# Performance work log

Hardware: AMD Instinct MI355X
Metric: run time of the kernel (lower is better)

Reference implementation:

```python
import jax, jax.numpy as jnp
import numpy as np

B, T, C = 1, 4096, 1024
N_HEAD = 16
HEAD_DIM = C // N_HEAD
SCALE = 1.0 / np.sqrt(HEAD_DIM).astype(np.float32)


def setup_inputs() -> dict:
    key = jax.random.key(0)
    k1, k2, k3 = jax.random.split(key, 3)
    x = jax.random.normal(k1, (B, T, C), dtype=jnp.float32)
    W_attn = jax.random.normal(k2, (C, 3 * C), dtype=jnp.float32) * 0.02
    b_attn = jnp.zeros((3 * C,), dtype=jnp.float32)
    W_proj = jax.random.normal(k3, (C, C), dtype=jnp.float32) * 0.02
    b_proj = jnp.zeros((C,), dtype=jnp.float32)
    return {"x": x, "W_attn": W_attn, "b_attn": b_attn, "W_proj": W_proj, "b_proj": b_proj}


def reference(x, W_attn, b_attn, W_proj, b_proj):
    Bq, Tq, Cq = x.shape
    qkv = x @ W_attn + b_attn                      # [B, T, 3C]
    q, k, v = jnp.split(qkv, 3, axis=-1)
    # split heads -> [B, H, T, D]
    def split_heads(t):
        return t.reshape(Bq, Tq, N_HEAD, HEAD_DIM).transpose(0, 2, 1, 3)
    q, k, v = split_heads(q), split_heads(k), split_heads(v)
    scores = jnp.einsum('bhqd,bhkd->bhqk', q, k) * SCALE  # [B, H, T, T]
    causal = jnp.tril(jnp.ones((Tq, Tq), dtype=bool))
    scores = jnp.where(causal[None, None], scores, jnp.float32(-jnp.inf))
    probs = jax.nn.softmax(scores, axis=-1)
    out = jnp.einsum('bhqk,bhkd->bhqd', probs, v)          # [B, H, T, D]
    out = out.transpose(0, 2, 1, 3).reshape(Bq, Tq, Cq)    # merge heads
    out = out @ W_proj + b_proj
    return out
```

## Files before the change

kernel.cpp:

```cpp
#include <hip/hip_runtime.h>
#include <hip/hip_bf16.h>


typedef unsigned short u16;
typedef u16 u16x4 __attribute__((ext_vector_type(4)));
typedef u16 u16x8 __attribute__((ext_vector_type(8)));
typedef __bf16 bf16x8 __attribute__((ext_vector_type(8)));
typedef float f32x4 __attribute__((ext_vector_type(4)));

#define T_SEQ 4096
#define C_DIM 1024
#define NH 16
#define HD 64
#define QSC 0.18033688f
#define NJOBS 1280

static __device__ __forceinline__ u16 f2bf(float f) {
    __hip_bfloat16 h = __float2bfloat16(f);
    return __builtin_bit_cast(u16, h);
}

static __device__ __forceinline__ bf16x8 ldfr(const u16* base, int byteoff) {
    return __builtin_bit_cast(bf16x8, *(const u16x8*)(base + (byteoff >> 1)));
}

static __device__ __forceinline__ void gld_lds16(const void* g, void* l) {
    __builtin_amdgcn_global_load_lds((const __attribute__((address_space(1))) void*)g,
                                     (__attribute__((address_space(3))) void*)l, 16, 0, 0);
}

#define MFMA16(a, b, c) __builtin_amdgcn_mfma_f32_16x16x32_bf16((a), (b), (c), 0, 0, 0)


__global__ __launch_bounds__(256) void k_cvt_x(const float* __restrict__ x, u16* __restrict__ xb) {
    int i = (blockIdx.x * 256 + threadIdx.x) * 8;
    float4 a = *(const float4*)(x + i);
    float4 b = *(const float4*)(x + i + 4);
    u16x8 o;
    o[0] = f2bf(a.x); o[1] = f2bf(a.y); o[2] = f2bf(a.z); o[3] = f2bf(a.w);
    o[4] = f2bf(b.x); o[5] = f2bf(b.y); o[6] = f2bf(b.z); o[7] = f2bf(b.w);
    *(u16x8*)(xb + i) = o;
}

__global__ __launch_bounds__(256) void k_transpose_w(const float* __restrict__ src,
                                                     u16* __restrict__ dst, int R, int Cc) {
    __shared__ float tile[32][33];
    int bx = blockIdx.x * 32;
    int by = blockIdx.y * 32;
    int x = threadIdx.x, y = threadIdx.y;
#pragma unroll
    for (int i = 0; i < 32; i += 8)
        tile[y + i][x] = src[(by + y + i) * Cc + bx + x];
    __syncthreads();
#pragma unroll
    for (int i = 0; i < 32; i += 8)
        dst[(bx + y + i) * R + by + x] = f2bf(tile[x][y + i]);
}


template <int EPI>
__global__ __launch_bounds__(256) void k_gemm(const u16* __restrict__ A, const u16* __restrict__ Bt,
                                              const float* __restrict__ bias,
                                              u16* __restrict__ outQ, u16* __restrict__ outK,
                                              u16* __restrict__ outVt, float* __restrict__ outF,
                                              int kd, int nbx) {
    __shared__ u16 Al[128 * 64];
    __shared__ u16 Bl[128 * 64];
    const int tid = threadIdx.x;
    const int lane = tid & 63;
    const int wid = tid >> 6;
    const int wm = wid >> 1, wn = wid & 1;
    const int c = lane & 15, g = lane >> 4;
    const int nwg = gridDim.x;
    const int swzb = ((int)blockIdx.x & 7) * (nwg >> 3) + ((int)blockIdx.x >> 3);
    const int m0 = (swzb % nbx) * 128;
    const int n0 = (swzb / nbx) * 128;
    const int srow = lane >> 3;
    const int sxu = (((lane & 7) * 16) ^ (srow << 4)) >> 1;
    const int swa = (c & 7) << 4;

    f32x4 acc[4][4] = {};

    for (int k0 = 0; k0 < kd; k0 += 64) {
#pragma unroll
        for (int i = 0; i < 4; ++i) {
            const int ch = wid * 4 + i;
            const int row = ch * 8 + srow;
            gld_lds16(A + (m0 + row) * kd + k0 + sxu, &Al[ch * 512]);
            gld_lds16(Bt + (n0 + row) * kd + k0 + sxu, &Bl[ch * 512]);
        }
        __syncthreads();
        bf16x8 af[4][2], bfm[4][2];
#pragma unroll
        for (int mi = 0; mi < 4; ++mi) {
            const u16* p = Al + (wm * 64 + mi * 16 + c) * 64;
            af[mi][0] = ldfr(p, (16 * g) ^ swa);
            af[mi][1] = ldfr(p, (64 + 16 * g) ^ swa);
        }
#pragma unroll
        for (int ni = 0; ni < 4; ++ni) {
            const u16* p = Bl + (wn * 64 + ni * 16 + c) * 64;
            bfm[ni][0] = ldfr(p, (16 * g) ^ swa);
            bfm[ni][1] = ldfr(p, (64 + 16 * g) ^ swa);
        }
#pragma unroll
        for (int mi = 0; mi < 4; ++mi)
#pragma unroll
            for (int ni = 0; ni < 4; ++ni) {
                acc[mi][ni] = MFMA16(af[mi][0], bfm[ni][0], acc[mi][ni]);
                acc[mi][ni] = MFMA16(af[mi][1], bfm[ni][1], acc[mi][ni]);
            }
        __syncthreads();
    }

    const int mbase = m0 + wm * 64;
    const int nbase = n0 + wn * 64;
    if (EPI == 0) {
        const int part = m0 >> 10;
#pragma unroll
        for (int mi = 0; mi < 4; ++mi) {
            const int fbase = mbase + mi * 16 + 4 * g;
            const f32x4 bv = *(const f32x4*)(bias + part * 1024 + (part ? fbase - part * 1024 + part * 1024 : fbase));
            const int fr = fbase & 1023;
            const int h = fr >> 6, d0 = fr & 63;
#pragma unroll
            for (int ni = 0; ni < 4; ++ni) {
                const int tok = nbase + ni * 16 + c;
                if (part == 2) {
#pragma unroll
                    for (int r = 0; r < 4; ++r)
                        outVt[(size_t)(fr + r) * T_SEQ + tok] = f2bf(acc[mi][ni][r] + bv[r]);
                } else {
                    u16x4 pk;
#pragma unroll
                    for (int r = 0; r < 4; ++r) {
                        float v = acc[mi][ni][r] + bv[r];
                        pk[r] = f2bf(part == 0 ? v * QSC : v);
                    }
                    u16* dst = (part == 0 ? outQ : outK);
                    *(u16x4*)(dst + (size_t)(h * T_SEQ + tok) * HD + d0) = pk;
                }
            }
        }
    } else {
#pragma unroll
        for (int mi = 0; mi < 4; ++mi) {
            const int fbase = mbase + mi * 16 + 4 * g;
            const f32x4 bv = *(const f32x4*)(bias + fbase);
#pragma unroll
            for (int ni = 0; ni < 4; ++ni) {
                const int tok = nbase + ni * 16 + c;
                f32x4 w;
#pragma unroll
                for (int r = 0; r < 4; ++r) w[r] = acc[mi][ni][r] + bv[r];
                *(f32x4*)(outF + (size_t)tok * C_DIM + fbase) = w;
            }
        }
    }
}


static __device__ __forceinline__ void p_gen(f32x4 s[4], int qabs, int kv0, int g,
                                             bool domask, bf16x8 pa[2]) {
    if (domask) {
#pragma unroll
        for (int tau = 0; tau < 4; ++tau) {
            const int kb = kv0 + 32 * (tau >> 1) + 4 * (tau & 1) + 8 * g;
#pragma unroll
            for (int r = 0; r < 4; ++r)
                if (kb + r > qabs) s[tau][r] = -3e38f;
        }
    }
    u16 pb[4][4];
#pragma unroll
    for (int tau = 0; tau < 4; ++tau)
#pragma unroll
        for (int r = 0; r < 4; ++r)
            pb[tau][r] = f2bf(__builtin_amdgcn_exp2f(s[tau][r]));
    const u16x8 p0 = {pb[0][0], pb[0][1], pb[0][2], pb[0][3], pb[1][0], pb[1][1], pb[1][2], pb[1][3]};
    const u16x8 p1 = {pb[2][0], pb[2][1], pb[2][2], pb[2][3], pb[3][0], pb[3][1], pb[3][2], pb[3][3]};
    pa[0] = __builtin_bit_cast(bf16x8, p0);
    pa[1] = __builtin_bit_cast(bf16x8, p1);
}

__global__ __launch_bounds__(256) void k_flash(const u16* __restrict__ Qg, const u16* __restrict__ Kg,
                                               const u16* __restrict__ Vtg,
                                               float* __restrict__ part, float* __restrict__ lpart,
                                               unsigned* __restrict__ cnt) {
    __shared__ u16 sm[2][2][4096];
    volatile unsigned* jw = (volatile unsigned*)&sm[0][0][0];

    const int tid = threadIdx.x;
    const int lane = tid & 63;
    const int wid = tid >> 6;
    const int c = lane & 15, g = lane >> 4;
    const int srow = lane >> 3;
    const int sxu = (((lane & 7) * 16) ^ (srow << 4)) >> 1;

    const u16x8 onespat = {0x3F80, 0x3F80, 0x3F80, 0x3F80, 0x3F80, 0x3F80, 0x3F80, 0x3F80};
    const bf16x8 onesf = __builtin_bit_cast(bf16x8, onespat);

    for (;;) {
        if (tid == 0) *jw = atomicAdd(cnt, 1u);
        __syncthreads();
        const unsigned j = *jw;
        __syncthreads();
        if (j >= (unsigned)NJOBS) break;

        const int head = (int)(j & 15u);
        const int idx = (int)(j >> 4);
        int qb, ch, nc;
        if (idx < 32)      { qb = 31 - (idx >> 2); ch = idx & 3; nc = 4; }
        else if (idx < 56) { const int t = idx - 32; qb = 23 - t / 3;    ch = t % 3; nc = 3; }
        else if (idx < 72) { const int t = idx - 56; qb = 15 - (t >> 1); ch = t & 1; nc = 2; }
        else               { qb = 7 - (idx - 72); ch = 0; nc = 1; }
        const int ntile = 2 * qb + 2;
        const int cbase = ntile / nc, crem = ntile % nc;
        const int len = cbase + (ch < crem ? 1 : 0);
        const int start = ch * cbase + (ch < crem ? ch : crem);

        const int q0w = qb * 128 + wid * 32;

        const u16* Qh = Qg + (size_t)head * (T_SEQ * HD);
        const u16* Kh = Kg + (size_t)head * (T_SEQ * HD);
        const u16* Vh = Vtg + (size_t)head * (HD * T_SEQ);

        bf16x8 qf[2][2];
#pragma unroll
        for (int h = 0; h < 2; ++h)
#pragma unroll
            for (int dc = 0; dc < 2; ++dc)
                qf[h][dc] = __builtin_bit_cast(
                    bf16x8, *(const u16x8*)(Qh + (q0w + 16 * h + c) * HD + dc * 32 + 8 * g));

        f32x4 o0[4] = {}, o1[4] = {}, ol0 = {}, ol1 = {};

        {
            const int kvs = start * 64;
#pragma unroll
            for (int i = 0; i < 2; ++i) {
                const int chk = wid * 2 + i;
                gld_lds16(Kh + (kvs + chk * 8 + srow) * HD + sxu, &sm[0][0][chk * 512]);
                gld_lds16(Vh + (chk * 8 + srow) * T_SEQ + kvs + sxu, &sm[0][1][chk * 512]);
            }
        }
        __syncthreads();

        for (int t = 0; t < len; ++t) {
            const int cur = t & 1;
            const int kv0 = (start + t) * 64;
            if (t + 1 < len) {
                const int kvn = kv0 + 64;
#pragma unroll
                for (int i = 0; i < 2; ++i) {
                    const int chk = wid * 2 + i;
                    gld_lds16(Kh + (kvn + chk * 8 + srow) * HD + sxu, &sm[cur ^ 1][0][chk * 512]);
                    gld_lds16(Vh + (chk * 8 + srow) * T_SEQ + kvn + sxu, &sm[cur ^ 1][1][chk * 512]);
                }
            }
            const u16* Kl = &sm[cur][0][0];
            const u16* Vl = &sm[cur][1][0];
            f32x4 s0[4], s1[4];
            __builtin_amdgcn_s_setprio(1);
#pragma unroll
            for (int tau = 0; tau < 4; ++tau) {
                const int prow = 32 * (tau >> 1) + 4 * (tau & 1) + 8 * (c >> 2) + (c & 3);
                const int sw = (prow & 7) << 4;
                const u16* kb = Kl + prow * 64;
                const bf16x8 k0 = ldfr(kb, (16 * g) ^ sw);
                const bf16x8 k1 = ldfr(kb, (64 + 16 * g) ^ sw);
                f32x4 z0 = {}, z1 = {};
                z0 = MFMA16(k0, qf[0][0], z0);
                s0[tau] = MFMA16(k1, qf[0][1], z0);
                z1 = MFMA16(k0, qf[1][0], z1);
                s1[tau] = MFMA16(k1, qf[1][1], z1);
            }
            __builtin_amdgcn_s_setprio(0);
            const bool dm0 = (kv0 + 63) > (q0w);
            const bool dm1 = (kv0 + 63) > (q0w + 16);
            bf16x8 pa0[2], pa1[2];
            p_gen(s0, q0w + c, kv0, g, dm0, pa0);
            p_gen(s1, q0w + 16 + c, kv0, g, dm1, pa1);
            const int swv = (c & 7) << 4;
            __builtin_amdgcn_s_setprio(1);
#pragma unroll
            for (int n = 0; n < 4; ++n) {
                const u16* vb = Vl + (n * 16 + c) * 64;
                const bf16x8 v0 = ldfr(vb, (16 * g) ^ swv);
                const bf16x8 v1 = ldfr(vb, (64 + 16 * g) ^ swv);
                o0[n] = MFMA16(v0, pa0[0], o0[n]);
                o0[n] = MFMA16(v1, pa0[1], o0[n]);
                o1[n] = MFMA16(v0, pa1[0], o1[n]);
                o1[n] = MFMA16(v1, pa1[1], o1[n]);
            }
            ol0 = MFMA16(onesf, pa0[0], ol0);
            ol0 = MFMA16(onesf, pa0[1], ol0);
            ol1 = MFMA16(onesf, pa1[0], ol1);
            ol1 = MFMA16(onesf, pa1[1], ol1);
            __builtin_amdgcn_s_setprio(0);
            __syncthreads();
        }

        float* slot = part + (size_t)j * 8192u;
        float* lsl = lpart + (size_t)j * 128u;
        const int ql0 = wid * 32 + c;
#pragma unroll
        for (int n = 0; n < 4; ++n) {
            *(f32x4*)(slot + ql0 * 64 + n * 16 + 4 * g) = o0[n];
            *(f32x4*)(slot + (ql0 + 16) * 64 + n * 16 + 4 * g) = o1[n];
        }
        if (g == 0) {
            lsl[ql0] = ol0[0];
            lsl[ql0 + 16] = ol1[0];
        }
        __syncthreads();
    }
}


__global__ __launch_bounds__(256) void k_combine(const float* __restrict__ part,
                                                 const float* __restrict__ lpart,
                                                 u16* __restrict__ Ab) {
    const int head = blockIdx.x >> 5, qb = blockIdx.x & 31;
    int nc, idx0;
    if (qb >= 24)      { nc = 4; idx0 = (31 - qb) * 4; }
    else if (qb >= 16) { nc = 3; idx0 = 32 + (23 - qb) * 3; }
    else if (qb >= 8)  { nc = 2; idx0 = 56 + (15 - qb) * 2; }
    else               { nc = 1; idx0 = 72 + (7 - qb); }

    const int q = threadIdx.x >> 1;
    const int dh = (threadIdx.x & 1) * 32;
    f32x4 a[8] = {};
    float l = 0.f;
    for (int i = 0; i < nc; ++i) {
        const unsigned jj = (unsigned)(((idx0 + i) << 4) | head);
        const float* sp = part + (size_t)jj * 8192u + q * 64 + dh;
#pragma unroll
        for (int r = 0; r < 8; ++r) a[r] += *(const f32x4*)(sp + 4 * r);
        l += lpart[(size_t)jj * 128u + q];
    }
    const float li = 1.0f / l;
    u16* dst = Ab + (size_t)(qb * 128 + q) * C_DIM + head * HD + dh;
#pragma unroll
    for (int v = 0; v < 4; ++v) {
        u16x8 w;
#pragma unroll
        for (int r = 0; r < 4; ++r) {
            w[r] = f2bf(a[2 * v][r] * li);
            w[r + 4] = f2bf(a[2 * v + 1][r] * li);
        }
        *(u16x8*)(dst + v * 8) = w;
    }
}


extern "C" void kernel_launch(void* const* d_in, const int* in_sizes, int n_in,
                              void* d_out, int out_size, void* d_ws, size_t ws_size,
                              hipStream_t stream) {
    const float* x      = (const float*)d_in[0];
    const float* W_attn = (const float*)d_in[1];
    const float* b_attn = (const float*)d_in[2];
    const float* W_proj = (const float*)d_in[3];
    const float* b_proj = (const float*)d_in[4];
    float* out = (float*)d_out;

    char* ws = (char*)d_ws;
    u16* xb    = (u16*)(ws);
    u16* Wat   = (u16*)(ws + (8u << 20));
    u16* Wpt   = (u16*)(ws + (14u << 20));
    u16* Qb    = (u16*)(ws + (16u << 20));
    u16* Kb    = (u16*)(ws + (24u << 20));
    u16* Vtb   = (u16*)(ws + (32u << 20));
    float* prt = (float*)(ws + (40u << 20));
    float* lpt = (float*)(ws + (80u << 20));
    u16* Ab    = xb;

    unsigned* cnt = (unsigned*)d_out;
    hipMemsetAsync(cnt, 0, 4, stream);

    k_cvt_x<<<2048, 256, 0, stream>>>(x, xb);
    k_transpose_w<<<dim3(96, 32), dim3(32, 8), 0, stream>>>(W_attn, Wat, 1024, 3072);
    k_transpose_w<<<dim3(32, 32), dim3(32, 8), 0, stream>>>(W_proj, Wpt, 1024, 1024);
    k_gemm<0><<<768, 256, 0, stream>>>(Wat, xb, b_attn, Qb, Kb, Vtb, nullptr, 1024, 24);
    k_flash<<<640, 256, 0, stream>>>(Qb, Kb, Vtb, prt, lpt, cnt);
    k_combine<<<512, 256, 0, stream>>>(prt, lpt, Ab);
    k_gemm<1><<<256, 256, 0, stream>>>(Wpt, Ab, b_proj, nullptr, nullptr, nullptr, out, 1024, 8);
}
```

Baseline: 166.2 us.

## Split flash attention into finer KV chunks and store bf16 partials

Raises the number of split-KV jobs from 1280 to 2304, using up to 8 chunks per query block, and doubles the persistent flash grid. The goal is better load balance and more work in flight across CUs. Partial outputs are now stored as bf16 instead of fp32, which halves the write and read traffic between the flash and combine kernels. In exchange, the combine step has more partials to sum, and rounding the unnormalized partials to bf16 adds precision loss. The bias indexing expression is also simplified.

```diff
diff --git a/kernel.cpp b/kernel.cpp
--- a/kernel.cpp
+++ b/kernel.cpp
@@ -13,11 +13,15 @@
 #define NH 16
 #define HD 64
 #define QSC 0.18033688f
-#define NJOBS 1280
+#define NJOBS 2304
 
 static __device__ __forceinline__ u16 f2bf(float f) {
     __hip_bfloat16 h = __float2bfloat16(f);
     return __builtin_bit_cast(u16, h);
+}
+
+static __device__ __forceinline__ float bf2f(u16 u) {
+    return __builtin_bit_cast(float, (unsigned)u << 16);
 }
 
 static __device__ __forceinline__ bf16x8 ldfr(const u16* base, int byteoff) {
@@ -120,7 +124,7 @@
 #pragma unroll
         for (int mi = 0; mi < 4; ++mi) {
             const int fbase = mbase + mi * 16 + 4 * g;
-            const f32x4 bv = *(const f32x4*)(bias + part * 1024 + (part ? fbase - part * 1024 + part * 1024 : fbase));
+            const f32x4 bv = *(const f32x4*)(bias + fbase);
             const int fr = fbase & 1023;
             const int h = fr >> 6, d0 = fr & 63;
 #pragma unroll
@@ -185,7 +189,7 @@
 
 __global__ __launch_bounds__(256) void k_flash(const u16* __restrict__ Qg, const u16* __restrict__ Kg,
                                                const u16* __restrict__ Vtg,
-                                               float* __restrict__ part, float* __restrict__ lpart,
+                                               u16* __restrict__ part, float* __restrict__ lpart,
                                                unsigned* __restrict__ cnt) {
     __shared__ u16 sm[2][2][4096];
     volatile unsigned* jw = (volatile unsigned*)&sm[0][0][0];
@@ -210,10 +214,14 @@
         const int head = (int)(j & 15u);
         const int idx = (int)(j >> 4);
         int qb, ch, nc;
-        if (idx < 32)      { qb = 31 - (idx >> 2); ch = idx & 3; nc = 4; }
-        else if (idx < 56) { const int t = idx - 32; qb = 23 - t / 3;    ch = t % 3; nc = 3; }
-        else if (idx < 72) { const int t = idx - 56; qb = 15 - (t >> 1); ch = t & 1; nc = 2; }
-        else               { qb = 7 - (idx - 72); ch = 0; nc = 1; }
+        if (idx < 32)       { qb = 31 - (idx >> 3); ch = idx & 7; nc = 8; }
+        else if (idx < 60)  { const int t = idx - 32;  qb = 27 - t / 7;    ch = t % 7; nc = 7; }
+        else if (idx < 84)  { const int t = idx - 60;  qb = 23 - t / 6;    ch = t % 6; nc = 6; }
+        else if (idx < 104) { const int t = idx - 84;  qb = 19 - t / 5;    ch = t % 5; nc = 5; }
+        else if (idx < 120) { const int t = idx - 104; qb = 15 - (t >> 2); ch = t & 3; nc = 4; }
+        else if (idx < 132) { const int t = idx - 120; qb = 11 - t / 3;    ch = t % 3; nc = 3; }
+        else if (idx < 140) { const int t = idx - 132; qb = 7 - (t >> 1);  ch = t & 1; nc = 2; }
+        else                { qb = 3 - (idx - 140); ch = 0; nc = 1; }
         const int ntile = 2 * qb + 2;
         const int cbase = ntile / nc, crem = ntile % nc;
         const int len = cbase + (ch < crem ? 1 : 0);
@@ -301,13 +309,19 @@
             __syncthreads();
         }
 
-        float* slot = part + (size_t)j * 8192u;
+        u16* slot = part + (size_t)j * 8192u;
         float* lsl = lpart + (size_t)j * 128u;
         const int ql0 = wid * 32 + c;
 #pragma unroll
         for (int n = 0; n < 4; ++n) {
-            *(f32x4*)(slot + ql0 * 64 + n * 16 + 4 * g) = o0[n];
-            *(f32x4*)(slot + (ql0 + 16) * 64 + n * 16 + 4 * g) = o1[n];
+            u16x4 w0, w1;
+#pragma unroll
+            for (int r = 0; r < 4; ++r) {
+                w0[r] = f2bf(o0[n][r]);
+                w1[r] = f2bf(o1[n][r]);
+            }
+            *(u16x4*)(slot + ql0 * 64 + n * 16 + 4 * g) = w0;
+            *(u16x4*)(slot + (ql0 + 16) * 64 + n * 16 + 4 * g) = w1;
         }
         if (g == 0) {
             lsl[ql0] = ol0[0];
@@ -318,25 +332,33 @@
 }
 
 
-__global__ __launch_bounds__(256) void k_combine(const float* __restrict__ part,
+__global__ __launch_bounds__(256) void k_combine(const u16* __restrict__ part,
                                                  const float* __restrict__ lpart,
                                                  u16* __restrict__ Ab) {
     const int head = blockIdx.x >> 5, qb = blockIdx.x & 31;
     int nc, idx0;
-    if (qb >= 24)      { nc = 4; idx0 = (31 - qb) * 4; }
-    else if (qb >= 16) { nc = 3; idx0 = 32 + (23 - qb) * 3; }
-    else if (qb >= 8)  { nc = 2; idx0 = 56 + (15 - qb) * 2; }
-    else               { nc = 1; idx0 = 72 + (7 - qb); }
+    if (qb >= 28)      { nc = 8; idx0 = (31 - qb) * 8; }
+    else if (qb >= 24) { nc = 7; idx0 = 32 + (27 - qb) * 7; }
+    else if (qb >= 20) { nc = 6; idx0 = 60 + (23 - qb) * 6; }
+    else if (qb >= 16) { nc = 5; idx0 = 84 + (19 - qb) * 5; }
+    else if (qb >= 12) { nc = 4; idx0 = 104 + (15 - qb) * 4; }
+    else if (qb >= 8)  { nc = 3; idx0 = 120 + (11 - qb) * 3; }
+    else if (qb >= 4)  { nc = 2; idx0 = 132 + (7 - qb) * 2; }
+    else               { nc = 1; idx0 = 140 + (3 - qb); }
 
     const int q = threadIdx.x >> 1;
     const int dh = (threadIdx.x & 1) * 32;
-    f32x4 a[8] = {};
+    float acc[32] = {};
     float l = 0.f;
     for (int i = 0; i < nc; ++i) {
         const unsigned jj = (unsigned)(((idx0 + i) << 4) | head);
-        const float* sp = part + (size_t)jj * 8192u + q * 64 + dh;
-#pragma unroll
-        for (int r = 0; r < 8; ++r) a[r] += *(const f32x4*)(sp + 4 * r);
+        const u16* sp = part + (size_t)jj * 8192u + q * 64 + dh;
+#pragma unroll
+        for (int v = 0; v < 4; ++v) {
+            const u16x8 w = *(const u16x8*)(sp + 8 * v);
+#pragma unroll
+            for (int e = 0; e < 8; ++e) acc[8 * v + e] += bf2f(w[e]);
+        }
         l += lpart[(size_t)jj * 128u + q];
     }
     const float li = 1.0f / l;
@@ -345,11 +367,8 @@
     for (int v = 0; v < 4; ++v) {
         u16x8 w;
 #pragma unroll
-        for (int r = 0; r < 4; ++r) {
-            w[r] = f2bf(a[2 * v][r] * li);
-            w[r + 4] = f2bf(a[2 * v + 1][r] * li);
-        }
-        *(u16x8*)(dst + v * 8) = w;
+        for (int e = 0; e < 8; ++e) w[e] = f2bf(acc[8 * v + e] * li);
+        *(u16x8*)(dst + 8 * v) = w;
     }
 }
 
@@ -371,8 +390,8 @@
     u16* Qb    = (u16*)(ws + (16u << 20));
     u16* Kb    = (u16*)(ws + (24u << 20));
     u16* Vtb   = (u16*)(ws + (32u << 20));
-    float* prt = (float*)(ws + (40u << 20));
-    float* lpt = (float*)(ws + (80u << 20));
+    u16* prt   = (u16*)(ws + (40u << 20));
+    float* lpt = (float*)(ws + (78u << 20));
     u16* Ab    = xb;
 
     unsigned* cnt = (unsigned*)d_out;
@@ -382,7 +401,7 @@
     k_transpose_w<<<dim3(96, 32), dim3(32, 8), 0, stream>>>(W_attn, Wat, 1024, 3072);
     k_transpose_w<<<dim3(32, 32), dim3(32, 8), 0, stream>>>(W_proj, Wpt, 1024, 1024);
     k_gemm<0><<<768, 256, 0, stream>>>(Wat, xb, b_attn, Qb, Kb, Vtb, nullptr, 1024, 24);
-    k_flash<<<640, 256, 0, stream>>>(Qb, Kb, Vtb, prt, lpt, cnt);
+    k_flash<<<1280, 256, 0, stream>>>(Qb, Kb, Vtb, prt, lpt, cnt);
     k_combine<<<512, 256, 0, stream>>>(prt, lpt, Ab);
     k_gemm<1><<<256, 256, 0, stream>>>(Wpt, Ab, b_proj, nullptr, nullptr, nullptr, out, 1024, 8);
 }
```

Result: slower. 172.4 us (+3.7%).
